# Optimization experiments

Measured on AMD Instinct MI355X. Metric: run time of the kernel, lower is better.

The kernel has to match this reference:

```python
import jax, jax.numpy as jnp
import numpy as np

B, T, C, L = 1024, 1024, 96, 32
BLANK = C - 1          # tf.compat.v1.nn.ctc_loss uses num_classes-1 as blank
S = 2 * L + 1          # extended label length (blanks interleaved)
NEG = -1e30            # log-space 'zero'


def setup_inputs() -> dict:
    key = jax.random.key(0)
    k1, k2 = jax.random.split(key)
    y_true = jax.random.randint(k1, (B, L), 0, BLANK).astype(jnp.int64)  # labels in [0, C-2]
    y_pred = jax.random.normal(k2, (B, T, C), dtype=jnp.float32)          # pre-softmax logits
    return {"y_true": y_true, "y_pred": y_pred}


def _ctc_loss(y_pred, y_true):
    # y_pred: [B,T,C] logits, y_true: [B,L] int labels. All lengths are full
    # (label_length = L, input_length = T), matching the layer's call().
    logp = jax.nn.log_softmax(y_pred, axis=-1)                   # [B,T,C]
    # extended labels: blank, l0, blank, l1, ..., blank  -> [B,S]
    ext = jnp.full((B, S), BLANK, dtype=jnp.int32).at[:, 1::2].set(y_true.astype(jnp.int32))
    # skip transition allowed where ext[s] != blank and ext[s] != ext[s-2]
    skip = jnp.concatenate(
        [jnp.zeros((B, 2), bool), (ext[:, 2:] != BLANK) & (ext[:, 2:] != ext[:, :-2])],
        axis=1)                                                  # [B,S]
    # per-time emission log-probs of extended labels: [T,B,S]
    lp_ext = jnp.take_along_axis(logp, ext[:, None, :], axis=2)  # [B,T,S]
    lp_ext = jnp.transpose(lp_ext, (1, 0, 2))                    # [T,B,S]

    alpha0 = (jnp.full((B, S), NEG, dtype=logp.dtype)
              .at[:, 0].set(lp_ext[0, :, 0])
              .at[:, 1].set(lp_ext[0, :, 1]))

    def step(alpha, lp_t):
        a_stay = alpha
        a_prev = jnp.concatenate([jnp.full((B, 1), NEG, alpha.dtype), alpha[:, :-1]], axis=1)
        a_skip = jnp.concatenate([jnp.full((B, 2), NEG, alpha.dtype), alpha[:, :-2]], axis=1)
        a_skip = jnp.where(skip, a_skip, NEG)
        m = jnp.maximum(jnp.maximum(a_stay, a_prev), a_skip)
        new = m + jnp.log(jnp.exp(a_stay - m) + jnp.exp(a_prev - m) + jnp.exp(a_skip - m))
        return new + lp_t, None

    alphaT, _ = jax.lax.scan(step, alpha0, lp_ext[1:])
    # total log-likelihood ends at last blank or last label
    end = jnp.stack([alphaT[:, S - 1], alphaT[:, S - 2]], axis=0)  # [2,B]
    loss = -jax.scipy.special.logsumexp(end, axis=0)               # [B]
    return loss[:, None]                                           # [B,1], as ctc_batch_cost


def reference(y_true, y_pred):
    return _ctc_loss(y_pred, y_true)
```

## Files before the change

kernel.cpp:

```cpp
#include <hip/hip_runtime.h>


#define NB 1024
#define NT 1024
#define NC 96
#define NL 32
#define NEGF (-1e30f)
#define CHUNK 32
#define NCHUNK (NT / CHUNK)
#define SLOTF 97
#define LOG2E 1.4426950408889634f
#define LN2   0.69314718055994531f

__device__ __forceinline__ float fexp2(float x) { return __builtin_amdgcn_exp2f(x); }
__device__ __forceinline__ float flog2(float x) { return __builtin_amdgcn_logf(x); }

template <int CTRL>
__device__ __forceinline__ float dpp_mov(float v) {
  return __int_as_float(__builtin_amdgcn_update_dpp(
      __float_as_int(v), __float_as_int(v), CTRL, 0xF, 0xF, false));
}
__device__ __forceinline__ float dpp_shr1(float oldv, float v) {
  return __int_as_float(__builtin_amdgcn_update_dpp(
      __float_as_int(oldv), __float_as_int(v), 0x138, 0xF, 0xF, false));
}
__device__ __forceinline__ float dpp_shl1(float oldv, float v) {
  return __int_as_float(__builtin_amdgcn_update_dpp(
      __float_as_int(oldv), __float_as_int(v), 0x130, 0xF, 0xF, false));
}

__global__ __launch_bounds__(256) void ctc_fused(const int* __restrict__ yt,
                                                 const float* __restrict__ yp,
                                                 float* __restrict__ out) {
  __shared__ float ring[2 * CHUNK * SLOTF];

  const int b = blockIdx.x;
  const int wid = threadIdx.x >> 6;
  const int lane = threadIdx.x & 63;

  const float* __restrict__ xrow = yp + (size_t)b * NT * NC;

  const int cw = b & 3;
  const bool is_cons = (wid == cw);
  const int pr = ((wid - cw + 4) & 3) - 1;

  int extc = 95;
  bool skipf = false;
  if (is_cons) {
    const int* lab = yt + b * NL;
    if ((lane & 1) == 0) {
      const int j = lane >> 1;
      extc = lab[j];
      skipf = (j > 0) && (extc != lab[j - 1]);
    }
  }

  const int rsel = lane >> 5;
  const int l32 = lane & 31;

  float UA[6][3], UB[6][3];

  auto load_regs = [&](float (&U)[6][3], int t0) {
    const float* rp = xrow + (size_t)(t0 + 2 * pr + rsel) * NC + l32;
#pragma unroll
    for (int jj = 0; jj < 6; ++jj) {
      if (pr + 3 * jj < 16) {
        U[jj][0] = rp[jj * 6 * NC + 0];
        U[jj][1] = rp[jj * 6 * NC + 32];
        U[jj][2] = rp[jj * 6 * NC + 64];
      }
    }
  };

  auto compute_store = [&](float (&U)[6][3], int cc) {
    float* wb = ring + (cc & 1) * (CHUNK * SLOTF) + (2 * pr + rsel) * SLOTF + l32;
#pragma unroll
    for (int jj = 0; jj < 6; ++jj) {
      if (pr + 3 * jj < 16) {
        const float u0 = U[jj][0] * LOG2E;
        const float u1 = U[jj][1] * LOG2E;
        const float u2 = U[jj][2] * LOG2E;
        float z = fexp2(u0) + fexp2(u1) + fexp2(u2);
        z += dpp_mov<0xB1>(z);
        z += dpp_mov<0x4E>(z);
        z += dpp_mov<0x124>(z);
        z += dpp_mov<0x128>(z);
        z += __shfl_xor(z, 16);
        const float lz = flog2(z);
        wb[jj * 6 * SLOTF + 0]  = u0 - lz;
        wb[jj * 6 * SLOTF + 32] = u1 - lz;
        wb[jj * 6 * SLOTF + 64] = u2 - lz;
      }
    }
  };

  float alpha = NEGF;
  float a0 = NEGF;

  auto lse_step = [&](float lp) {
    const float blk = dpp_shl1(lp, lp);
    const float ap = dpp_shr1(a0, alpha);
    float as = dpp_shr1(NEGF, ap);
    as = skipf ? as : NEGF;
    const float mm = fmaxf(fmaxf(alpha, ap), as);
    const float sm = fexp2(alpha - mm) + fexp2(ap - mm) + fexp2(as - mm);
    alpha = mm + flog2(sm) + lp;
    a0 += blk;
  };

  auto consume = [&](int cc, bool first) {
    const float* hb = ring + (cc & 1) * (CHUNK * SLOTF) + extc;
    float lq[4];
    lq[0] = hb[0 * SLOTF];
    lq[1] = hb[1 * SLOTF];
    lq[2] = hb[2 * SLOTF];
    lq[3] = 0.0f;
#pragma unroll
    for (int tt = 0; tt < CHUNK; ++tt) {
      const float lp = lq[tt & 3];
      if (tt + 3 < CHUNK) lq[(tt + 3) & 3] = hb[(tt + 3) * SLOTF];
      if (first && tt == 0) {
        a0 = dpp_shl1(lp, lp);
        alpha = (lane == 0) ? lp : NEGF;
      } else {
        lse_step(lp);
      }
    }
  };

  if (!is_cons) load_regs(UA, 0);

  for (int c = 0; c < NCHUNK; c += 2) {
    if (!is_cons) {
      if (c + 1 < NCHUNK) load_regs(UB, (c + 1) * CHUNK);
      compute_store(UA, c);
      __syncthreads();
      if (c + 2 < NCHUNK) load_regs(UA, (c + 2) * CHUNK);
      compute_store(UB, c + 1);
      __syncthreads();
    } else {
      __syncthreads();
      if (c == 0) consume(0, true);
      else consume(c, false);
      __syncthreads();
      consume(c + 1, false);
    }
  }

  if (is_cons) {
    const float aS1 = __shfl(alpha, 63);
    const float aS2 = __shfl(alpha, 62);
    if (lane == 0) {
      const float mF = fmaxf(aS1, aS2);
      const float r = mF + flog2(fexp2(aS1 - mF) + fexp2(aS2 - mF));
      out[b] = -r * LN2;
    }
  }
}

extern "C" void kernel_launch(void* const* d_in, const int* in_sizes, int n_in,
                              void* d_out, int out_size, void* d_ws, size_t ws_size,
                              hipStream_t stream) {
  const int* yt = (const int*)d_in[0];
  const float* yp = (const float*)d_in[1];
  float* out = (float*)d_out;
  hipLaunchKernelGGL(ctc_fused, dim3(NB), dim3(256), 0, stream, yt, yp, out);
}
```

Measured before the change: 95.67 us.

## Replace log-space CTC recursion with mantissa/exponent scaled linear-space arithmetic

The producer now writes softmax probabilities (exp times reciprocal of the sum) instead of log-probabilities. The consumer runs the alpha recursion in linear space, keeping each value as a mantissa plus an integer exponent and aligning terms with ldexp and frexp. This removes the per-step exp2/log2 transcendentals on the serial critical path and replaces them with integer max, ldexp and frexp operations. The prefetch depth of the emission values is also widened. The risk is precision loss from adding values whose exponents differ widely, and added integer work on each step.

```diff
diff --git a/kernel.cpp b/kernel.cpp
--- a/kernel.cpp
+++ b/kernel.cpp
@@ -1,19 +1,28 @@
 #include <hip/hip_runtime.h>
+#include <limits.h>
 
 
 #define NB 1024
 #define NT 1024
 #define NC 96
 #define NL 32
-#define NEGF (-1e30f)
 #define CHUNK 32
 #define NCHUNK (NT / CHUNK)
 #define SLOTF 97
 #define LOG2E 1.4426950408889634f
 #define LN2   0.69314718055994531f
+#define DEADK (INT_MIN / 2)
 
 __device__ __forceinline__ float fexp2(float x) { return __builtin_amdgcn_exp2f(x); }
 __device__ __forceinline__ float flog2(float x) { return __builtin_amdgcn_logf(x); }
+__device__ __forceinline__ float frcp(float x)  { return __builtin_amdgcn_rcpf(x); }
+__device__ __forceinline__ float fmant(float x) { return __builtin_amdgcn_frexp_mantf(x); }
+__device__ __forceinline__ int   fexpo(float x) { return __builtin_amdgcn_frexp_expf(x); }
+__device__ __forceinline__ float fldexp(float x, int e) {
+  float r;
+  asm("v_ldexp_f32 %0, %1, %2" : "=v"(r) : "v"(x), "v"(e));
+  return r;
+}
 
 template <int CTRL>
 __device__ __forceinline__ float dpp_mov(float v) {
@@ -23,6 +32,9 @@
 __device__ __forceinline__ float dpp_shr1(float oldv, float v) {
   return __int_as_float(__builtin_amdgcn_update_dpp(
       __float_as_int(oldv), __float_as_int(v), 0x138, 0xF, 0xF, false));
+}
+__device__ __forceinline__ int dpp_shr1_i(int oldv, int v) {
+  return __builtin_amdgcn_update_dpp(oldv, v, 0x138, 0xF, 0xF, false);
 }
 __device__ __forceinline__ float dpp_shl1(float oldv, float v) {
   return __int_as_float(__builtin_amdgcn_update_dpp(
@@ -77,53 +89,65 @@
 #pragma unroll
     for (int jj = 0; jj < 6; ++jj) {
       if (pr + 3 * jj < 16) {
-        const float u0 = U[jj][0] * LOG2E;
-        const float u1 = U[jj][1] * LOG2E;
-        const float u2 = U[jj][2] * LOG2E;
-        float z = fexp2(u0) + fexp2(u1) + fexp2(u2);
+        const float e0 = fexp2(U[jj][0] * LOG2E);
+        const float e1 = fexp2(U[jj][1] * LOG2E);
+        const float e2 = fexp2(U[jj][2] * LOG2E);
+        float z = e0 + e1 + e2;
         z += dpp_mov<0xB1>(z);
         z += dpp_mov<0x4E>(z);
         z += dpp_mov<0x124>(z);
         z += dpp_mov<0x128>(z);
         z += __shfl_xor(z, 16);
-        const float lz = flog2(z);
-        wb[jj * 6 * SLOTF + 0]  = u0 - lz;
-        wb[jj * 6 * SLOTF + 32] = u1 - lz;
-        wb[jj * 6 * SLOTF + 64] = u2 - lz;
+        const float rz = frcp(z);
+        wb[jj * 6 * SLOTF + 0]  = e0 * rz;
+        wb[jj * 6 * SLOTF + 32] = e1 * rz;
+        wb[jj * 6 * SLOTF + 64] = e2 * rz;
       }
     }
   };
 
-  float alpha = NEGF;
-  float a0 = NEGF;
-
-  auto lse_step = [&](float lp) {
-    const float blk = dpp_shl1(lp, lp);
-    const float ap = dpp_shr1(a0, alpha);
-    float as = dpp_shr1(NEGF, ap);
-    as = skipf ? as : NEGF;
-    const float mm = fmaxf(fmaxf(alpha, ap), as);
-    const float sm = fexp2(alpha - mm) + fexp2(ap - mm) + fexp2(as - mm);
-    alpha = mm + flog2(sm) + lp;
-    a0 += blk;
-  };
+  float va = 0.0f;
+  int ka = DEADK;
+  float va0 = 0.0f;
+  int k0 = DEADK;
 
   auto consume = [&](int cc, bool first) {
     const float* hb = ring + (cc & 1) * (CHUNK * SLOTF) + extc;
-    float lq[4];
-    lq[0] = hb[0 * SLOTF];
-    lq[1] = hb[1 * SLOTF];
-    lq[2] = hb[2 * SLOTF];
-    lq[3] = 0.0f;
+    float lq[8];
+#pragma unroll
+    for (int i = 0; i < 6; i += 2) {
+      lq[i] = hb[i * SLOTF];
+      lq[i + 1] = hb[(i + 1) * SLOTF];
+    }
 #pragma unroll
     for (int tt = 0; tt < CHUNK; ++tt) {
-      const float lp = lq[tt & 3];
-      if (tt + 3 < CHUNK) lq[(tt + 3) & 3] = hb[(tt + 3) * SLOTF];
+      const float lp = lq[tt & 7];
+      if ((tt & 1) == 0 && tt + 7 < CHUNK) {
+        const float* p2 = hb + (tt + 6) * SLOTF;
+        lq[(tt + 6) & 7] = p2[0];
+        lq[(tt + 7) & 7] = p2[SLOTF];
+      }
+      const float pb = dpp_shl1(lp, lp);
       if (first && tt == 0) {
-        a0 = dpp_shl1(lp, lp);
-        alpha = (lane == 0) ? lp : NEGF;
+        va0 = pb; k0 = 0;
+        va = (lane == 0) ? lp : 0.0f;
+        ka = (lane == 0) ? 0 : DEADK;
       } else {
-        lse_step(lp);
+        const float vap = dpp_shr1(va0, va);
+        const int kap = dpp_shr1_i(k0, ka);
+        float vas = dpp_shr1(0.0f, vap);
+        int kas = dpp_shr1_i(DEADK, kap);
+        vas = skipf ? vas : 0.0f;
+        kas = skipf ? kas : DEADK;
+        const int kref = max(max(ka, kap), kas);
+        float s = fldexp(va, ka - kref) + fldexp(vap, kap - kref) +
+                  fldexp(vas, kas - kref);
+        s *= lp;
+        ka = kref + fexpo(s);
+        va = fmant(s);
+        va0 *= pb;
+        k0 += fexpo(va0);
+        va0 = fmant(va0);
       }
     }
   };
@@ -148,12 +172,14 @@
   }
 
   if (is_cons) {
-    const float aS1 = __shfl(alpha, 63);
-    const float aS2 = __shfl(alpha, 62);
+    const float v1 = __shfl(va, 63);
+    const int e1 = __shfl(ka, 63);
+    const float v2 = __shfl(va, 62);
+    const int e2 = __shfl(ka, 62);
     if (lane == 0) {
-      const float mF = fmaxf(aS1, aS2);
-      const float r = mF + flog2(fexp2(aS1 - mF) + fexp2(aS2 - mF));
-      out[b] = -r * LN2;
+      const int kref = max(e1, e2);
+      const float s = fldexp(v1, e1 - kref) + fldexp(v2, e2 - kref);
+      out[b] = -(flog2(s) + (float)kref) * LN2;
     }
   }
 }
```

New measurement: 134.5 us. +40.6%, slower.
